# Kernel tuning notes

Measured on AMD Instinct MI355X. Metric: run time of the kernel, lower is better.

The kernel has to match this reference:

```python
import jax, jax.numpy as jnp
import numpy as np

B, N, D = 8192, 512, 3

def setup_inputs() -> dict:
    key = jax.random.key(0)
    k1, k2 = jax.random.split(key)
    inp = jax.random.normal(k1, (B, N, D), dtype=jnp.float32)
    tgt = jax.random.normal(k2, (B, N, D), dtype=jnp.float32)
    return {"input": inp, "target": tgt}

def _kabsch_rotation(x, y):
    # x, y: (B, N, 3) centered. Covariance C: (B, 3, 3)
    C = jnp.einsum('bji,bjk->bik', x, y)
    U, _, Vh = jnp.linalg.svd(C, full_matrices=False)
    d = jnp.linalg.det(U) * jnp.linalg.det(Vh)  # (B,)
    # flip sign of last row of Vh where det is negative (proper rotation)
    Vh = Vh.at[:, -1, :].multiply(d[:, None])
    return U @ Vh  # (B, 3, 3)

def reference(input, target):
    x = input - input.mean(-2, keepdims=True)
    y = target - target.mean(-2, keepdims=True)
    R = _kabsch_rotation(x, y)
    aligned = jnp.einsum('bnd,bde->bne', x, R)
    return jnp.mean((aligned - y) ** 2)
```

## Files before the change

### kernel.cpp

```cpp
#include <hip/hip_runtime.h>
#include <math.h>

#define B_TOT 8192
#define N_PTS 512
#define WAVES_PER_BLOCK 4
#define BLK_A (64 * WAVES_PER_BLOCK)

struct f3 { float x, y, z; };

__device__ __forceinline__ float dpp_wave_sum(float v) {
    int x;
    x = __builtin_amdgcn_update_dpp(0, __float_as_int(v), 0x111, 0xF, 0xF, true);
    v += __int_as_float(x);
    x = __builtin_amdgcn_update_dpp(0, __float_as_int(v), 0x112, 0xF, 0xF, true);
    v += __int_as_float(x);
    x = __builtin_amdgcn_update_dpp(0, __float_as_int(v), 0x114, 0xF, 0xF, true);
    v += __int_as_float(x);
    x = __builtin_amdgcn_update_dpp(0, __float_as_int(v), 0x118, 0xF, 0xF, true);
    v += __int_as_float(x);
    x = __builtin_amdgcn_update_dpp(0, __float_as_int(v), 0x142, 0xF, 0xF, true);
    v += __int_as_float(x);
    x = __builtin_amdgcn_update_dpp(0, __float_as_int(v), 0x143, 0xF, 0xF, true);
    v += __int_as_float(x);
    return v;
}

__global__ __launch_bounds__(BLK_A) void sums_kernel(const float* __restrict__ x,
                                                     const float* __restrict__ y,
                                                     float* __restrict__ ws,
                                                     double* __restrict__ acc_out,
                                                     unsigned* __restrict__ cnt)
{
    if (blockIdx.x == 0 && threadIdx.x == 0) { *acc_out = 0.0; *cnt = 0u; }

    const int wave = threadIdx.x >> 6;
    const int lane = threadIdx.x & 63;
    const int b = blockIdx.x * WAVES_PER_BLOCK + wave;

    const f3* __restrict__ xb = reinterpret_cast<const f3*>(x) + (size_t)b * N_PTS;
    const f3* __restrict__ yb = reinterpret_cast<const f3*>(y) + (size_t)b * N_PTS;

    float a[17];
    #pragma unroll
    for (int k = 0; k < 17; k++) a[k] = 0.f;

    #pragma unroll
    for (int p = 0; p < 8; p++) {
        f3 X = xb[p * 64 + lane];
        f3 Y = yb[p * 64 + lane];
        a[0] += X.x;  a[1] += X.y;  a[2] += X.z;
        a[3] += Y.x;  a[4] += Y.y;  a[5] += Y.z;
        a[6]  += X.x*Y.x; a[7]  += X.x*Y.y; a[8]  += X.x*Y.z;
        a[9]  += X.y*Y.x; a[10] += X.y*Y.y; a[11] += X.y*Y.z;
        a[12] += X.z*Y.x; a[13] += X.z*Y.y; a[14] += X.z*Y.z;
        a[15] += X.x*X.x + X.y*X.y + X.z*X.z;
        a[16] += Y.x*Y.x + Y.y*Y.y + Y.z*Y.z;
    }

    #pragma unroll
    for (int k = 0; k < 17; k++) a[k] = dpp_wave_sum(a[k]);

    if (lane == 63) {
        #pragma unroll
        for (int k = 0; k < 17; k++) ws[k * B_TOT + b] = a[k];
    }
}

__global__ __launch_bounds__(256) void solve_kernel(const float* __restrict__ ws,
                                                    double* __restrict__ acc_out,
                                                    unsigned* __restrict__ cnt,
                                                    float* __restrict__ out)
{
    const int b = blockIdx.x * 256 + threadIdx.x;

    double S[17];
    #pragma unroll
    for (int k = 0; k < 17; k++) S[k] = (double)ws[k * B_TOT + b];

    const double Nn = (double)N_PTS;
    double mx[3] = {S[0]/Nn, S[1]/Nn, S[2]/Nn};
    double my[3] = {S[3]/Nn, S[4]/Nn, S[5]/Nn};

    double C[3][3];
    #pragma unroll
    for (int d = 0; d < 3; d++)
        #pragma unroll
        for (int e = 0; e < 3; e++)
            C[d][e] = S[6 + d*3 + e] - Nn * mx[d] * my[e];

    double sxx = S[15] - Nn*(mx[0]*mx[0] + mx[1]*mx[1] + mx[2]*mx[2]);
    double syy = S[16] - Nn*(my[0]*my[0] + my[1]*my[1] + my[2]*my[2]);

    double K00=0,K01=0,K02=0,K11=0,K12=0,K22=0;
    #pragma unroll
    for (int k = 0; k < 3; k++) {
        K00 += C[k][0]*C[k][0]; K01 += C[k][0]*C[k][1]; K02 += C[k][0]*C[k][2];
        K11 += C[k][1]*C[k][1]; K12 += C[k][1]*C[k][2]; K22 += C[k][2]*C[k][2];
    }

    double q3 = (K00 + K11 + K22) / 3.0;
    double p1 = K01*K01 + K02*K02 + K12*K12;
    double a00 = K00 - q3, a11 = K11 - q3, a22 = K22 - q3;
    double p2 = a00*a00 + a11*a11 + a22*a22 + 2.0*p1;
    double lam1, lam2, lam3;
    if (p2 <= 1e-300) {
        lam1 = lam2 = lam3 = q3;
    } else {
        double pp  = sqrt(p2 / 6.0);
        double ip  = 1.0 / pp;
        double b00 = a00*ip, b11 = a11*ip, b22 = a22*ip;
        double b01 = K01*ip, b02 = K02*ip, b12 = K12*ip;
        double detB = b00*(b11*b22 - b12*b12)
                    - b01*(b01*b22 - b12*b02)
                    + b02*(b01*b12 - b11*b02);
        double r = 0.5 * detB;
        r = fmin(1.0, fmax(-1.0, r));
        double phi = acos(r) / 3.0;
        lam1 = q3 + 2.0*pp*cos(phi);
        lam3 = q3 + 2.0*pp*cos(phi + 2.0943951023931954923);
        lam2 = 3.0*q3 - lam1 - lam3;
    }
    lam1 = fmax(lam1, 0.0); lam2 = fmax(lam2, 0.0); lam3 = fmax(lam3, 0.0);
    double s1 = sqrt(lam1), s2 = sqrt(lam2), s3 = sqrt(lam3);

    double detC = C[0][0]*(C[1][1]*C[2][2] - C[1][2]*C[2][1])
                - C[0][1]*(C[1][0]*C[2][2] - C[1][2]*C[2][0])
                + C[0][2]*(C[1][0]*C[2][1] - C[1][1]*C[2][0]);
    double sgn = (detC < 0.0) ? -1.0 : 1.0;
    double trRC = s1 + s2 + sgn * s3;

    double v = sxx + syy - 2.0 * trRC;

    #pragma unroll
    for (int off = 32; off; off >>= 1) v += __shfl_down(v, off, 64);
    __shared__ double red[4];
    const int wave = threadIdx.x >> 6, lane = threadIdx.x & 63;
    if (lane == 0) red[wave] = v;
    __syncthreads();

    if (threadIdx.x == 0) {
        double blk = red[0] + red[1] + red[2] + red[3];
        atomicAdd(acc_out, blk);
        __threadfence();
        unsigned t = atomicAdd(cnt, 1u);
        if (t == gridDim.x - 1) {
            __threadfence();
            double total = atomicAdd(acc_out, 0.0);
            out[0] = (float)(total / ((double)B_TOT * (double)N_PTS * 3.0));
        }
    }
}

extern "C" void kernel_launch(void* const* d_in, const int* in_sizes, int n_in,
                              void* d_out, int out_size, void* d_ws, size_t ws_size,
                              hipStream_t stream) {
    const float* x = (const float*)d_in[0];
    const float* y = (const float*)d_in[1];
    float* out = (float*)d_out;

    float*    ws  = (float*)d_ws;
    double*   acc = (double*)((char*)d_ws + 17 * B_TOT * 4);
    unsigned* cnt = (unsigned*)((char*)d_ws + 17 * B_TOT * 4 + 8);

    sums_kernel <<<B_TOT / WAVES_PER_BLOCK, BLK_A, 0, stream>>>(x, y, ws, acc, cnt);
    solve_kernel<<<B_TOT / 256, 256, 0, stream>>>(ws, acc, cnt, out);
}
```

Baseline: 116.7 us.

## Fuse per-batch Kabsch solve into sums kernel and use single-block final reduction

Moves the per-batch closed-form eigenvalue/trace computation into the sums kernel, where lane 63 of each wave solves its batch directly and the block writes one partial sum. This removes the 17-float-per-batch workspace round trip and the global atomic/counter reduction. A single-block final kernel sums the 2048 partials deterministically. The cost is that the double-precision solve now runs on one lane per wave inside the bandwidth-bound kernel, leaving 63 lanes idle during it.

```diff
diff --git a/kernel.cpp b/kernel.cpp
--- a/kernel.cpp
+++ b/kernel.cpp
@@ -5,6 +5,7 @@
 #define N_PTS 512
 #define WAVES_PER_BLOCK 4
 #define BLK_A (64 * WAVES_PER_BLOCK)
+#define GRID_A (B_TOT / WAVES_PER_BLOCK)
 
 struct f3 { float x, y, z; };
 
@@ -25,14 +26,10 @@
     return v;
 }
 
-__global__ __launch_bounds__(BLK_A) void sums_kernel(const float* __restrict__ x,
-                                                     const float* __restrict__ y,
-                                                     float* __restrict__ ws,
-                                                     double* __restrict__ acc_out,
-                                                     unsigned* __restrict__ cnt)
+__global__ __launch_bounds__(BLK_A) void fused_kernel(const float* __restrict__ x,
+                                                      const float* __restrict__ y,
+                                                      double* __restrict__ blockSums)
 {
-    if (blockIdx.x == 0 && threadIdx.x == 0) { *acc_out = 0.0; *cnt = 0u; }
-
     const int wave = threadIdx.x >> 6;
     const int lane = threadIdx.x & 63;
     const int b = blockIdx.x * WAVES_PER_BLOCK + wave;
@@ -60,95 +57,92 @@
     #pragma unroll
     for (int k = 0; k < 17; k++) a[k] = dpp_wave_sum(a[k]);
 
+    double v = 0.0;
     if (lane == 63) {
+        double S[17];
         #pragma unroll
-        for (int k = 0; k < 17; k++) ws[k * B_TOT + b] = a[k];
+        for (int k = 0; k < 17; k++) S[k] = (double)a[k];
+
+        const double Nn = (double)N_PTS;
+        double mx[3] = {S[0]/Nn, S[1]/Nn, S[2]/Nn};
+        double my[3] = {S[3]/Nn, S[4]/Nn, S[5]/Nn};
+
+        double C[3][3];
+        #pragma unroll
+        for (int d = 0; d < 3; d++)
+            #pragma unroll
+            for (int e = 0; e < 3; e++)
+                C[d][e] = S[6 + d*3 + e] - Nn * mx[d] * my[e];
+
+        double sxx = S[15] - Nn*(mx[0]*mx[0] + mx[1]*mx[1] + mx[2]*mx[2]);
+        double syy = S[16] - Nn*(my[0]*my[0] + my[1]*my[1] + my[2]*my[2]);
+
+        double K00=0,K01=0,K02=0,K11=0,K12=0,K22=0;
+        #pragma unroll
+        for (int k = 0; k < 3; k++) {
+            K00 += C[k][0]*C[k][0]; K01 += C[k][0]*C[k][1]; K02 += C[k][0]*C[k][2];
+            K11 += C[k][1]*C[k][1]; K12 += C[k][1]*C[k][2]; K22 += C[k][2]*C[k][2];
+        }
+
+        double q3 = (K00 + K11 + K22) / 3.0;
+        double p1 = K01*K01 + K02*K02 + K12*K12;
+        double a00 = K00 - q3, a11 = K11 - q3, a22 = K22 - q3;
+        double p2 = a00*a00 + a11*a11 + a22*a22 + 2.0*p1;
+        double lam1, lam2, lam3;
+        if (p2 <= 1e-300) {
+            lam1 = lam2 = lam3 = q3;
+        } else {
+            double pp  = sqrt(p2 / 6.0);
+            double ip  = 1.0 / pp;
+            double b00 = a00*ip, b11 = a11*ip, b22 = a22*ip;
+            double b01 = K01*ip, b02 = K02*ip, b12 = K12*ip;
+            double detB = b00*(b11*b22 - b12*b12)
+                        - b01*(b01*b22 - b12*b02)
+                        + b02*(b01*b12 - b11*b02);
+            double r = 0.5 * detB;
+            r = fmin(1.0, fmax(-1.0, r));
+            double phi = acos(r) / 3.0;
+            lam1 = q3 + 2.0*pp*cos(phi);
+            lam3 = q3 + 2.0*pp*cos(phi + 2.0943951023931954923);
+            lam2 = 3.0*q3 - lam1 - lam3;
+        }
+        lam1 = fmax(lam1, 0.0); lam2 = fmax(lam2, 0.0); lam3 = fmax(lam3, 0.0);
+        double s1 = sqrt(lam1), s2 = sqrt(lam2), s3 = sqrt(lam3);
+
+        double detC = C[0][0]*(C[1][1]*C[2][2] - C[1][2]*C[2][1])
+                    - C[0][1]*(C[1][0]*C[2][2] - C[1][2]*C[2][0])
+                    + C[0][2]*(C[1][0]*C[2][1] - C[1][1]*C[2][0]);
+        double sgn = (detC < 0.0) ? -1.0 : 1.0;
+        double trRC = s1 + s2 + sgn * s3;
+
+        v = sxx + syy - 2.0 * trRC;
     }
+
+    __shared__ double red[WAVES_PER_BLOCK];
+    if (lane == 63) red[wave] = v;
+    __syncthreads();
+    if (threadIdx.x == 0)
+        blockSums[blockIdx.x] = red[0] + red[1] + red[2] + red[3];
 }
 
-__global__ __launch_bounds__(256) void solve_kernel(const float* __restrict__ ws,
-                                                    double* __restrict__ acc_out,
-                                                    unsigned* __restrict__ cnt,
+__global__ __launch_bounds__(256) void final_kernel(const double* __restrict__ bs,
                                                     float* __restrict__ out)
 {
-    const int b = blockIdx.x * 256 + threadIdx.x;
-
-    double S[17];
+    double v = 0.0;
     #pragma unroll
-    for (int k = 0; k < 17; k++) S[k] = (double)ws[k * B_TOT + b];
-
-    const double Nn = (double)N_PTS;
-    double mx[3] = {S[0]/Nn, S[1]/Nn, S[2]/Nn};
-    double my[3] = {S[3]/Nn, S[4]/Nn, S[5]/Nn};
-
-    double C[3][3];
-    #pragma unroll
-    for (int d = 0; d < 3; d++)
-        #pragma unroll
-        for (int e = 0; e < 3; e++)
-            C[d][e] = S[6 + d*3 + e] - Nn * mx[d] * my[e];
-
-    double sxx = S[15] - Nn*(mx[0]*mx[0] + mx[1]*mx[1] + mx[2]*mx[2]);
-    double syy = S[16] - Nn*(my[0]*my[0] + my[1]*my[1] + my[2]*my[2]);
-
-    double K00=0,K01=0,K02=0,K11=0,K12=0,K22=0;
-    #pragma unroll
-    for (int k = 0; k < 3; k++) {
-        K00 += C[k][0]*C[k][0]; K01 += C[k][0]*C[k][1]; K02 += C[k][0]*C[k][2];
-        K11 += C[k][1]*C[k][1]; K12 += C[k][1]*C[k][2]; K22 += C[k][2]*C[k][2];
-    }
-
-    double q3 = (K00 + K11 + K22) / 3.0;
-    double p1 = K01*K01 + K02*K02 + K12*K12;
-    double a00 = K00 - q3, a11 = K11 - q3, a22 = K22 - q3;
-    double p2 = a00*a00 + a11*a11 + a22*a22 + 2.0*p1;
-    double lam1, lam2, lam3;
-    if (p2 <= 1e-300) {
-        lam1 = lam2 = lam3 = q3;
-    } else {
-        double pp  = sqrt(p2 / 6.0);
-        double ip  = 1.0 / pp;
-        double b00 = a00*ip, b11 = a11*ip, b22 = a22*ip;
-        double b01 = K01*ip, b02 = K02*ip, b12 = K12*ip;
-        double detB = b00*(b11*b22 - b12*b12)
-                    - b01*(b01*b22 - b12*b02)
-                    + b02*(b01*b12 - b11*b02);
-        double r = 0.5 * detB;
-        r = fmin(1.0, fmax(-1.0, r));
-        double phi = acos(r) / 3.0;
-        lam1 = q3 + 2.0*pp*cos(phi);
-        lam3 = q3 + 2.0*pp*cos(phi + 2.0943951023931954923);
-        lam2 = 3.0*q3 - lam1 - lam3;
-    }
-    lam1 = fmax(lam1, 0.0); lam2 = fmax(lam2, 0.0); lam3 = fmax(lam3, 0.0);
-    double s1 = sqrt(lam1), s2 = sqrt(lam2), s3 = sqrt(lam3);
-
-    double detC = C[0][0]*(C[1][1]*C[2][2] - C[1][2]*C[2][1])
-                - C[0][1]*(C[1][0]*C[2][2] - C[1][2]*C[2][0])
-                + C[0][2]*(C[1][0]*C[2][1] - C[1][1]*C[2][0]);
-    double sgn = (detC < 0.0) ? -1.0 : 1.0;
-    double trRC = s1 + s2 + sgn * s3;
-
-    double v = sxx + syy - 2.0 * trRC;
+    for (int i = 0; i < GRID_A / 256; i++)
+        v += bs[i * 256 + threadIdx.x];
 
     #pragma unroll
     for (int off = 32; off; off >>= 1) v += __shfl_down(v, off, 64);
+
     __shared__ double red[4];
     const int wave = threadIdx.x >> 6, lane = threadIdx.x & 63;
     if (lane == 0) red[wave] = v;
     __syncthreads();
-
-    if (threadIdx.x == 0) {
-        double blk = red[0] + red[1] + red[2] + red[3];
-        atomicAdd(acc_out, blk);
-        __threadfence();
-        unsigned t = atomicAdd(cnt, 1u);
-        if (t == gridDim.x - 1) {
-            __threadfence();
-            double total = atomicAdd(acc_out, 0.0);
-            out[0] = (float)(total / ((double)B_TOT * (double)N_PTS * 3.0));
-        }
-    }
+    if (threadIdx.x == 0)
+        out[0] = (float)((red[0] + red[1] + red[2] + red[3])
+                         / ((double)B_TOT * (double)N_PTS * 3.0));
 }
 
 extern "C" void kernel_launch(void* const* d_in, const int* in_sizes, int n_in,
@@ -158,10 +152,8 @@
     const float* y = (const float*)d_in[1];
     float* out = (float*)d_out;
 
-    float*    ws  = (float*)d_ws;
-    double*   acc = (double*)((char*)d_ws + 17 * B_TOT * 4);
-    unsigned* cnt = (unsigned*)((char*)d_ws + 17 * B_TOT * 4 + 8);
+    double* bs = (double*)d_ws;
 
-    sums_kernel <<<B_TOT / WAVES_PER_BLOCK, BLK_A, 0, stream>>>(x, y, ws, acc, cnt);
-    solve_kernel<<<B_TOT / 256, 256, 0, stream>>>(ws, acc, cnt, out);
+    fused_kernel<<<GRID_A, BLK_A, 0, stream>>>(x, y, bs);
+    final_kernel<<<1, 256, 0, stream>>>(bs, out);
 }
```

Measured after the change: 117.9 us. No clear change (+1.1%).

## Fuse reduction and Kabsch solve into one kernel, two batches per wave

Applied to the files above, without the earlier changes.

Merges the per-batch moment reduction and the closed-form Kabsch solve into a single kernel, removing the intermediate workspace round-trip and the second launch. Each wave now handles two batches and the solve runs on two lanes, one per batch. Accumulator reset moves to a hipMemsetAsync. This halves the grid and serialises the solve inside each wave, so there is less parallelism across waves and a lane-serial double-precision tail per wave.

```diff
diff --git a/kernel.cpp b/kernel.cpp
--- a/kernel.cpp
+++ b/kernel.cpp
@@ -5,6 +5,7 @@
 #define N_PTS 512
 #define WAVES_PER_BLOCK 4
 #define BLK_A (64 * WAVES_PER_BLOCK)
+#define GRID_A (B_TOT / (2 * WAVES_PER_BLOCK))
 
 struct f3 { float x, y, z; };
 
@@ -25,58 +26,17 @@
     return v;
 }
 
-__global__ __launch_bounds__(BLK_A) void sums_kernel(const float* __restrict__ x,
-                                                     const float* __restrict__ y,
-                                                     float* __restrict__ ws,
-                                                     double* __restrict__ acc_out,
-                                                     unsigned* __restrict__ cnt)
-{
-    if (blockIdx.x == 0 && threadIdx.x == 0) { *acc_out = 0.0; *cnt = 0u; }
-
-    const int wave = threadIdx.x >> 6;
-    const int lane = threadIdx.x & 63;
-    const int b = blockIdx.x * WAVES_PER_BLOCK + wave;
-
-    const f3* __restrict__ xb = reinterpret_cast<const f3*>(x) + (size_t)b * N_PTS;
-    const f3* __restrict__ yb = reinterpret_cast<const f3*>(y) + (size_t)b * N_PTS;
-
-    float a[17];
-    #pragma unroll
-    for (int k = 0; k < 17; k++) a[k] = 0.f;
-
-    #pragma unroll
-    for (int p = 0; p < 8; p++) {
-        f3 X = xb[p * 64 + lane];
-        f3 Y = yb[p * 64 + lane];
-        a[0] += X.x;  a[1] += X.y;  a[2] += X.z;
-        a[3] += Y.x;  a[4] += Y.y;  a[5] += Y.z;
-        a[6]  += X.x*Y.x; a[7]  += X.x*Y.y; a[8]  += X.x*Y.z;
-        a[9]  += X.y*Y.x; a[10] += X.y*Y.y; a[11] += X.y*Y.z;
-        a[12] += X.z*Y.x; a[13] += X.z*Y.y; a[14] += X.z*Y.z;
-        a[15] += X.x*X.x + X.y*X.y + X.z*X.z;
-        a[16] += Y.x*Y.x + Y.y*Y.y + Y.z*Y.z;
-    }
-
-    #pragma unroll
-    for (int k = 0; k < 17; k++) a[k] = dpp_wave_sum(a[k]);
-
-    if (lane == 63) {
-        #pragma unroll
-        for (int k = 0; k < 17; k++) ws[k * B_TOT + b] = a[k];
-    }
+__device__ __forceinline__ void accum17(float* a, const f3& X, const f3& Y) {
+    a[0] += X.x;  a[1] += X.y;  a[2] += X.z;
+    a[3] += Y.x;  a[4] += Y.y;  a[5] += Y.z;
+    a[6]  += X.x*Y.x; a[7]  += X.x*Y.y; a[8]  += X.x*Y.z;
+    a[9]  += X.y*Y.x; a[10] += X.y*Y.y; a[11] += X.y*Y.z;
+    a[12] += X.z*Y.x; a[13] += X.z*Y.y; a[14] += X.z*Y.z;
+    a[15] += X.x*X.x + X.y*X.y + X.z*X.z;
+    a[16] += Y.x*Y.x + Y.y*Y.y + Y.z*Y.z;
 }
 
-__global__ __launch_bounds__(256) void solve_kernel(const float* __restrict__ ws,
-                                                    double* __restrict__ acc_out,
-                                                    unsigned* __restrict__ cnt,
-                                                    float* __restrict__ out)
-{
-    const int b = blockIdx.x * 256 + threadIdx.x;
-
-    double S[17];
-    #pragma unroll
-    for (int k = 0; k < 17; k++) S[k] = (double)ws[k * B_TOT + b];
-
+__device__ __forceinline__ double kabsch_v(const double* S) {
     const double Nn = (double)N_PTS;
     double mx[3] = {S[0]/Nn, S[1]/Nn, S[2]/Nn};
     double my[3] = {S[3]/Nn, S[4]/Nn, S[5]/Nn};
@@ -129,13 +89,59 @@
     double sgn = (detC < 0.0) ? -1.0 : 1.0;
     double trRC = s1 + s2 + sgn * s3;
 
-    double v = sxx + syy - 2.0 * trRC;
+    return sxx + syy - 2.0 * trRC;
+}
+
+__global__ __launch_bounds__(BLK_A) void fused_kernel(const float* __restrict__ x,
+                                                      const float* __restrict__ y,
+                                                      double* __restrict__ acc_out,
+                                                      unsigned* __restrict__ cnt,
+                                                      float* __restrict__ out)
+{
+    const int wave = threadIdx.x >> 6;
+    const int lane = threadIdx.x & 63;
+    const int pair = blockIdx.x * WAVES_PER_BLOCK + wave;
+
+    const f3* __restrict__ xb = reinterpret_cast<const f3*>(x) + (size_t)pair * 2 * N_PTS;
+    const f3* __restrict__ yb = reinterpret_cast<const f3*>(y) + (size_t)pair * 2 * N_PTS;
+
+    float aA[17], aB[17];
+    #pragma unroll
+    for (int k = 0; k < 17; k++) { aA[k] = 0.f; aB[k] = 0.f; }
 
     #pragma unroll
-    for (int off = 32; off; off >>= 1) v += __shfl_down(v, off, 64);
-    __shared__ double red[4];
-    const int wave = threadIdx.x >> 6, lane = threadIdx.x & 63;
-    if (lane == 0) red[wave] = v;
+    for (int p = 0; p < 8; p++) {
+        f3 X = xb[p * 64 + lane];
+        f3 Y = yb[p * 64 + lane];
+        accum17(aA, X, Y);
+    }
+    #pragma unroll
+    for (int p = 8; p < 16; p++) {
+        f3 X = xb[p * 64 + lane];
+        f3 Y = yb[p * 64 + lane];
+        accum17(aB, X, Y);
+    }
+
+    #pragma unroll
+    for (int k = 0; k < 17; k++) { aA[k] = dpp_wave_sum(aA[k]); aB[k] = dpp_wave_sum(aB[k]); }
+
+    float sB[17];
+    #pragma unroll
+    for (int k = 0; k < 17; k++) sB[k] = __shfl(aB[k], 63, 64);
+
+    double v = 0.0;
+    if (lane >= 62) {
+        double S[17];
+        #pragma unroll
+        for (int k = 0; k < 17; k++)
+            S[k] = (lane == 63) ? (double)aA[k] : (double)sB[k];
+        v = kabsch_v(S);
+    }
+
+    double vsum = v + __shfl_down(v, 1, 64);
+
+    __shared__ double red[WAVES_PER_BLOCK];
+    if (lane == 62) red[wave] = vsum;
     __syncthreads();
 
     if (threadIdx.x == 0) {
@@ -158,10 +164,9 @@
     const float* y = (const float*)d_in[1];
     float* out = (float*)d_out;
 
-    float*    ws  = (float*)d_ws;
-    double*   acc = (double*)((char*)d_ws + 17 * B_TOT * 4);
-    unsigned* cnt = (unsigned*)((char*)d_ws + 17 * B_TOT * 4 + 8);
+    double*   acc = (double*)d_ws;
+    unsigned* cnt = (unsigned*)((char*)d_ws + 8);
 
-    sums_kernel <<<B_TOT / WAVES_PER_BLOCK, BLK_A, 0, stream>>>(x, y, ws, acc, cnt);
-    solve_kernel<<<B_TOT / 256, 256, 0, stream>>>(ws, acc, cnt, out);
+    hipMemsetAsync(d_ws, 0, 16, stream);
+    fused_kernel<<<GRID_A, BLK_A, 0, stream>>>(x, y, acc, cnt, out);
 }
```

Result: slower. 161.4 us (+38.3%).
